# Optimization experiments

Hardware: AMD Instinct MI355X
Metric: run time of the kernel (lower is better)

Reference implementation:

```python
import jax, jax.numpy as jnp
import numpy as np

BATCH, SEQ, STATE, LATENT, ENC = 32, 2048, 64, 128, 256
INPUT_DIM = STATE + 2 * LATENT  # 320
BN_EPS = 1e-5


def setup_inputs() -> dict:
    key = jax.random.key(0)
    ks = jax.random.split(key, 16)
    def lin(k, fan_in, shape):
        b = 1.0 / np.sqrt(fan_in)
        return jax.random.uniform(k, shape, jnp.float32, -b, b)
    return {
        "padded_input": jax.random.normal(ks[0], (BATCH, SEQ, INPUT_DIM), jnp.float32),
        # encoder: state->enc, enc->enc, enc->latent (weights in (in,out) layout)
        "enc_w0": lin(ks[1], STATE, (STATE, ENC)),   "enc_b0": lin(ks[2], STATE, (ENC,)),
        "enc_w1": lin(ks[3], ENC, (ENC, ENC)),       "enc_b1": lin(ks[4], ENC, (ENC,)),
        "enc_w2": lin(ks[5], ENC, (ENC, LATENT)),    "enc_b2": lin(ks[6], ENC, (LATENT,)),
        "bn_gamma": jnp.ones((LATENT,), jnp.float32),
        "bn_beta": jnp.zeros((LATENT,), jnp.float32),
        "A_w": lin(ks[7], LATENT, (LATENT, LATENT)),  # A(x) = x @ A_w (no bias)
        "B_diag": (2.0 * jax.random.uniform(ks[8], (LATENT,), jnp.float32) - 1.0) * 0.8,
        # decoder: latent->enc, enc->enc, enc->state
        "dec_w0": lin(ks[9], LATENT, (LATENT, ENC)), "dec_b0": lin(ks[10], LATENT, (ENC,)),
        "dec_w1": lin(ks[11], ENC, (ENC, ENC)),      "dec_b1": lin(ks[12], ENC, (ENC,)),
        "dec_w2": lin(ks[13], ENC, (ENC, STATE)),    "dec_b2": lin(ks[14], ENC, (STATE,)),
        "reset_probability": 0,
        "nwarmup": 0,
    }


def reference(padded_input, enc_w0, enc_b0, enc_w1, enc_b1, enc_w2, enc_b2,
              bn_gamma, bn_beta, A_w, B_diag,
              dec_w0, dec_b0, dec_w1, dec_b1, dec_w2, dec_b2,
              reset_probability, nwarmup):
    state_dim = dec_w2.shape[1]
    latent = A_w.shape[0]
    x_t = padded_input[:, :, :state_dim]                       # [B,S,state]
    u_t1 = padded_input[:, :, state_dim + latent:]             # [B,S,latent]

    # encoder MLP (all ReLU)
    h = jax.nn.relu(x_t @ enc_w0 + enc_b0)
    h = jax.nn.relu(h @ enc_w1 + enc_b1)
    z = jax.nn.relu(h @ enc_w2 + enc_b2)                       # [B,S,latent]

    # BatchNorm1d (training mode): per-channel stats over batch and time
    mean = jnp.mean(z, axis=(0, 1))
    var = jnp.mean((z - mean) ** 2, axis=(0, 1))
    z = (z - mean) * jax.lax.rsqrt(var + BN_EPS) * bn_gamma + bn_beta

    # linear recurrence: z_0 = A z_enc[:,0] + B u_0 ; z_t = A z_{t-1} + B u_t
    d = jnp.clip(B_diag, -0.95, 0.95)
    bu = jnp.swapaxes(u_t1 * d, 0, 1)                          # [S,B,latent]

    def step(hprev, bu_t):
        hnew = hprev @ A_w + bu_t
        return hnew, hnew

    _, zs = jax.lax.scan(step, z[:, 0, :], bu)                 # [S,B,latent]
    z1 = jnp.swapaxes(zs, 0, 1)                                # [B,S,latent]

    # decoder MLP (ReLU except last)
    g = jax.nn.relu(z1 @ dec_w0 + dec_b0)
    g = jax.nn.relu(g @ dec_w1 + dec_b1)
    x_t1 = g @ dec_w2 + dec_b2                                 # [B,S,state]
    return x_t1
```

## Files before the change

### kernel.cpp

```cpp
#include <hip/hip_runtime.h>

#define DI __device__ __forceinline__

typedef __attribute__((ext_vector_type(8))) short short8;
typedef __attribute__((ext_vector_type(4))) float f32x4;
typedef unsigned short u16;
typedef unsigned int u32;

DI u16 f2bf(float f) {
  union { float f; u32 u; } v; v.f = f;
  u32 r = v.u + 0x7FFFu + ((v.u >> 16) & 1u);
  return (u16)(r >> 16);
}
DI float bf2f(u16 h) {
  union { u32 u; float f; } v; v.u = ((u32)h) << 16; return v.f;
}
DI f32x4 mfma16(short8 a, short8 b, f32x4 c) {
  return __builtin_amdgcn_mfma_f32_16x16x32_bf16(a, b, c, 0, 0, 0);
}


static const size_t OFF_HB   = 0;
static const size_t OFF_LB   = 16777216;
static const size_t OFF_WT   = 33554432;
static const size_t OFF_POWR = 34013184;
static const size_t OFF_POWT = 35127296;
static const size_t OFF_ST   = 35684352;
static const size_t OFF_ZB0  = 35685376;
static const size_t OFF_YB   = 35693568;
static const size_t OFF_INS  = 37790720;

#define OW0 0
#define OW1 16384
#define OW2 81920
#define OD0 114688
#define OD1 147456
#define OD2 212992

__global__ __launch_bounds__(256) void convw_k(const float* __restrict__ ew0, const float* __restrict__ ew1,
                                               const float* __restrict__ ew2, const float* __restrict__ dw0,
                                               const float* __restrict__ dw1, const float* __restrict__ dw2,
                                               const float* __restrict__ Aw, u16* __restrict__ wt,
                                               float* __restrict__ powR, u16* __restrict__ powT) {
  int idx = blockIdx.x * 256 + threadIdx.x;
  if (idx < 16384) { int n = idx >> 6, k = idx & 63;  wt[OW0 + idx] = f2bf(ew0[k * 256 + n]); return; }
  idx -= 16384;
  if (idx < 65536) { int n = idx >> 8, k = idx & 255; wt[OW1 + idx] = f2bf(ew1[k * 256 + n]); return; }
  idx -= 65536;
  if (idx < 32768) { int n = idx >> 8, k = idx & 255; wt[OW2 + idx] = f2bf(ew2[k * 128 + n]); return; }
  idx -= 32768;
  if (idx < 32768) { int n = idx >> 7, k = idx & 127; wt[OD0 + idx] = f2bf(dw0[k * 256 + n]); return; }
  idx -= 32768;
  if (idx < 65536) { int n = idx >> 8, k = idx & 255; wt[OD1 + idx] = f2bf(dw1[k * 256 + n]); return; }
  idx -= 65536;
  if (idx < 16384) { int n = idx >> 8, k = idx & 255; wt[OD2 + idx] = f2bf(dw2[k * 64 + n]); return; }
  idx -= 16384;
  { int k = idx >> 7, n = idx & 127;
    powR[16384 + idx] = Aw[idx];
    powT[16384 + n * 128 + k] = f2bf(Aw[idx]); }
}

template <int K, int KP, int NTW>
DI void layer(const u16* __restrict__ A, const u16* __restrict__ WT, int n0, int lm, int lq,
              f32x4 (&acc)[2][NTW]) {
  constexpr int KS = K / 32;
  constexpr int H = (KS > 4) ? 2 : 1;
  constexpr int KSH = KS / H;
#pragma unroll
  for (int h = 0; h < H; h++) {
    short8 bfr[NTW][KSH];
#pragma unroll
    for (int nt = 0; nt < NTW; nt++)
#pragma unroll
      for (int ks = 0; ks < KSH; ks++)
        bfr[nt][ks] = *(const short8*)&WT[(size_t)(n0 + nt * 16 + lm) * K + (h * KSH + ks) * 32 + lq * 8];
#pragma unroll
    for (int ks = 0; ks < KSH; ks++) {
      const int k0 = (h * KSH + ks) * 32 + lq * 8;
      short8 a0 = *(const short8*)&A[(0 * 16 + lm) * KP + k0];
      short8 a1 = *(const short8*)&A[(1 * 16 + lm) * KP + k0];
#pragma unroll
      for (int nt = 0; nt < NTW; nt++) {
        acc[0][nt] = mfma16(a0, bfr[nt][ks], acc[0][nt]);
        acc[1][nt] = mfma16(a1, bfr[nt][ks], acc[1][nt]);
      }
    }
  }
}

__global__ __launch_bounds__(256) void enc_k(const float* __restrict__ in, const u16* __restrict__ wt,
                                             const float* __restrict__ b0, const float* __restrict__ b1,
                                             const float* __restrict__ b2, float* __restrict__ st,
                                             u16* __restrict__ zb0) {
  __shared__ __align__(16) u16 bufA[32 * 264];
  __shared__ __align__(16) u16 bufB[32 * 264];
  __shared__ float sSum[128], sSq[128];
  const int tid = threadIdx.x, w = tid >> 6, l = tid & 63, lm = l & 15, lq = l >> 4;
  const int m0 = blockIdx.x * 32;
#pragma unroll
  for (int it = 0; it < 2; it++) {
    int idx = tid + it * 256;
    int row = idx >> 4, c4 = idx & 15;
    float4 f = *(const float4*)&in[(size_t)(m0 + row) * 320 + c4 * 4];
    u32 lo = (u32)f2bf(f.x) | ((u32)f2bf(f.y) << 16);
    u32 hi = (u32)f2bf(f.z) | ((u32)f2bf(f.w) << 16);
    *(uint2*)&bufA[row * 72 + c4 * 4] = make_uint2(lo, hi);
  }
  __syncthreads();
  {
    f32x4 acc[2][4];
#pragma unroll
    for (int i = 0; i < 2; i++)
#pragma unroll
      for (int j = 0; j < 4; j++) acc[i][j] = (f32x4){0.f, 0.f, 0.f, 0.f};
    layer<64, 72, 4>(bufA, wt + OW0, w * 64, lm, lq, acc);
#pragma unroll
    for (int nt = 0; nt < 4; nt++) {
      const int n = w * 64 + nt * 16 + lm;
      const float bv = b0[n];
#pragma unroll
      for (int mt = 0; mt < 2; mt++)
#pragma unroll
        for (int r = 0; r < 4; r++) {
          const int m = mt * 16 + lq * 4 + r;
          bufB[m * 264 + n] = f2bf(fmaxf(acc[mt][nt][r] + bv, 0.f));
        }
    }
  }
  __syncthreads();
  {
    f32x4 acc[2][4];
#pragma unroll
    for (int i = 0; i < 2; i++)
#pragma unroll
      for (int j = 0; j < 4; j++) acc[i][j] = (f32x4){0.f, 0.f, 0.f, 0.f};
    layer<256, 264, 4>(bufB, wt + OW1, w * 64, lm, lq, acc);
#pragma unroll
    for (int nt = 0; nt < 4; nt++) {
      const int n = w * 64 + nt * 16 + lm;
      const float bv = b1[n];
#pragma unroll
      for (int mt = 0; mt < 2; mt++)
#pragma unroll
        for (int r = 0; r < 4; r++) {
          const int m = mt * 16 + lq * 4 + r;
          bufA[m * 264 + n] = f2bf(fmaxf(acc[mt][nt][r] + bv, 0.f));
        }
    }
  }
  __syncthreads();
  {
    f32x4 acc[2][2];
#pragma unroll
    for (int i = 0; i < 2; i++)
#pragma unroll
      for (int j = 0; j < 2; j++) acc[i][j] = (f32x4){0.f, 0.f, 0.f, 0.f};
    layer<256, 264, 2>(bufA, wt + OW2, w * 32, lm, lq, acc);
    const bool t0blk = ((m0 & 2047) == 0);
#pragma unroll
    for (int nt = 0; nt < 2; nt++) {
      const int n = w * 32 + nt * 16 + lm;
      const float bv = b2[n];
      float sl = 0.f, sq = 0.f, r0v = 0.f;
#pragma unroll
      for (int mt = 0; mt < 2; mt++)
#pragma unroll
        for (int r = 0; r < 4; r++) {
          float v = fmaxf(acc[mt][nt][r] + bv, 0.f);
          sl += v; sq += v * v;
          if (mt == 0 && r == 0) r0v = v;
        }
      sl += __shfl_xor(sl, 16); sl += __shfl_xor(sl, 32);
      sq += __shfl_xor(sq, 16); sq += __shfl_xor(sq, 32);
      if (lq == 0) {
        sSum[n] = sl; sSq[n] = sq;
        if (t0blk) zb0[(m0 >> 11) * 128 + n] = f2bf(r0v);
      }
    }
  }
  __syncthreads();
  if (tid < 128) atomicAdd(&st[tid], sSum[tid]);
  else atomicAdd(&st[tid], sSq[tid - 128]);
}

__global__ __launch_bounds__(256) void dec_k(const u16* __restrict__ hb, const u16* __restrict__ wt,
                                             const float* __restrict__ b0, const float* __restrict__ b1,
                                             const float* __restrict__ b2, float* __restrict__ out) {
  __shared__ __align__(16) u16 bufA[32 * 264];
  __shared__ __align__(16) u16 bufB[32 * 264];
  const int tid = threadIdx.x, w = tid >> 6, l = tid & 63, lm = l & 15, lq = l >> 4;
  const int m0 = blockIdx.x * 32;
  for (int i = tid; i < 512; i += 256) {
    int row = i >> 4, c8 = i & 15;
    *(uint4*)&bufA[row * 136 + c8 * 8] = *(const uint4*)&hb[(size_t)(m0 + row) * 128 + c8 * 8];
  }
  __syncthreads();
  {
    f32x4 acc[2][4];
#pragma unroll
    for (int i = 0; i < 2; i++)
#pragma unroll
      for (int j = 0; j < 4; j++) acc[i][j] = (f32x4){0.f, 0.f, 0.f, 0.f};
    layer<128, 136, 4>(bufA, wt + OD0, w * 64, lm, lq, acc);
#pragma unroll
    for (int nt = 0; nt < 4; nt++) {
      const int n = w * 64 + nt * 16 + lm;
      const float bv = b0[n];
#pragma unroll
      for (int mt = 0; mt < 2; mt++)
#pragma unroll
        for (int r = 0; r < 4; r++) {
          const int m = mt * 16 + lq * 4 + r;
          bufB[m * 264 + n] = f2bf(fmaxf(acc[mt][nt][r] + bv, 0.f));
        }
    }
  }
  __syncthreads();
  {
    f32x4 acc[2][4];
#pragma unroll
    for (int i = 0; i < 2; i++)
#pragma unroll
      for (int j = 0; j < 4; j++) acc[i][j] = (f32x4){0.f, 0.f, 0.f, 0.f};
    layer<256, 264, 4>(bufB, wt + OD1, w * 64, lm, lq, acc);
#pragma unroll
    for (int nt = 0; nt < 4; nt++) {
      const int n = w * 64 + nt * 16 + lm;
      const float bv = b1[n];
#pragma unroll
      for (int mt = 0; mt < 2; mt++)
#pragma unroll
        for (int r = 0; r < 4; r++) {
          const int m = mt * 16 + lq * 4 + r;
          bufA[m * 264 + n] = f2bf(fmaxf(acc[mt][nt][r] + bv, 0.f));
        }
    }
  }
  __syncthreads();
  {
    f32x4 acc[2][1];
    acc[0][0] = (f32x4){0.f, 0.f, 0.f, 0.f};
    acc[1][0] = (f32x4){0.f, 0.f, 0.f, 0.f};
    layer<256, 264, 1>(bufA, wt + OD2, w * 16, lm, lq, acc);
    const int n = w * 16 + lm;
    const float bv = b2[n];
#pragma unroll
    for (int mt = 0; mt < 2; mt++)
#pragma unroll
      for (int r = 0; r < 4; r++) {
        const int m = mt * 16 + lq * 4 + r;
        out[(size_t)(m0 + m) * 64 + n] = acc[mt][0][r] + bv;
      }
  }
}

__global__ __launch_bounds__(128) void finalize_k(const float* __restrict__ st, const u16* __restrict__ zb0,
                                                  const float* __restrict__ gam, const float* __restrict__ bet,
                                                  u16* __restrict__ yb) {
  const int ch = threadIdx.x;
  const float mean = st[ch] * (1.f / 65536.f);
  const float var = st[128 + ch] * (1.f / 65536.f) - mean * mean;
  const float sc = rsqrtf(var + 1e-5f) * gam[ch];
  const float sh = bet[ch] - mean * sc;
  for (int b = 0; b < 32; b++) {
    float z = bf2f(zb0[b * 128 + ch]);
    yb[b * 128 + ch] = f2bf(z * sc + sh);
  }
}

__global__ __launch_bounds__(256) void pow_round_k(float* __restrict__ powR, u16* __restrict__ powT,
                                                   int p, int mi_base) {
  const int mi = mi_base + (blockIdx.x >> 2), nc = blockIdx.x & 3;
  const float* Rp = powR + (size_t)p * 16384;
  const float* Rm = powR + (size_t)(mi + 1) * 16384;
  float* Ro = powR + (size_t)(p + mi + 1) * 16384;
  u16* To = powT + (size_t)(p + mi + 1) * 16384;
  __shared__ __align__(16) float RpS[128 * 132];
  __shared__ __align__(16) float RmS[128 * 36];
  const int tid = threadIdx.x;
  for (int i = tid; i < 4096; i += 256) {
    int r = i >> 5, c4 = i & 31;
    *(float4*)&RpS[r * 132 + c4 * 4] = *(const float4*)&Rp[r * 128 + c4 * 4];
  }
  for (int i = tid; i < 1024; i += 256) {
    int r = i >> 3, c4 = i & 7;
    *(float4*)&RmS[r * 36 + c4 * 4] = *(const float4*)&Rm[r * 128 + nc * 32 + c4 * 4];
  }
  __syncthreads();
  const int tc = tid & 7, tr = tid >> 3;
  float acc[4][4];
#pragma unroll
  for (int i = 0; i < 4; i++)
#pragma unroll
    for (int j = 0; j < 4; j++) acc[i][j] = 0.f;
  for (int kk = 0; kk < 128; kk++) {
    const float4 bv = *(const float4*)&RmS[kk * 36 + tc * 4];
#pragma unroll
    for (int i = 0; i < 4; i++) {
      const float av = RpS[(tr * 4 + i) * 132 + kk];
      acc[i][0] += av * bv.x; acc[i][1] += av * bv.y;
      acc[i][2] += av * bv.z; acc[i][3] += av * bv.w;
    }
  }
#pragma unroll
  for (int i = 0; i < 4; i++)
#pragma unroll
    for (int j = 0; j < 4; j++) {
      const int row = tr * 4 + i, col = nc * 32 + tc * 4 + j;
      Ro[row * 128 + col] = acc[i][j];
      To[col * 128 + row] = f2bf(acc[i][j]);
    }
}

__global__ __launch_bounds__(256) void phase1_k(const float* __restrict__ in, const float* __restrict__ Bd,
                                                const u16* __restrict__ powT, u16* __restrict__ lb,
                                                u16* __restrict__ yb) {
  __shared__ __align__(16) u16 hS[2][32 * 136];
  __shared__ __align__(16) u16 buS[32 * 136];
  const int tid = threadIdx.x, c = blockIdx.x;
  const int w = tid >> 6, l = tid & 63, lm = l & 15, lq = l >> 4;
  const u16* T1 = powT + 16384;
  short8 bfr[2][4];
#pragma unroll
  for (int nt = 0; nt < 2; nt++)
#pragma unroll
    for (int ks = 0; ks < 4; ks++) {
      int n = (w * 2 + nt) * 16 + lm, k0 = ks * 32 + lq * 8;
      bfr[nt][ks] = *(const short8*)&T1[n * 128 + k0];
    }
  const int r0 = tid >> 4, ch = tid & 15;
  float dv[8];
#pragma unroll
  for (int j = 0; j < 8; j++) {
    float d = Bd[ch * 8 + j];
    dv[j] = fminf(0.95f, fmaxf(-0.95f, d));
  }
  const float* u0 = in + (size_t)r0 * 2048 * 320 + (size_t)(c * 8) * 320 + 192 + ch * 8;
  const float* u1 = in + (size_t)(r0 + 16) * 2048 * 320 + (size_t)(c * 8) * 320 + 192 + ch * 8;
  float4 p0 = *(const float4*)u0, p0b = *(const float4*)(u0 + 4);
  float4 p1 = *(const float4*)u1, p1b = *(const float4*)(u1 + 4);
  for (int tau = 0; tau < 8; tau++) {
    const int t = c * 8 + tau;
    short8 s0, s1;
    s0[0] = (short)f2bf(p0.x * dv[0]); s0[1] = (short)f2bf(p0.y * dv[1]);
    s0[2] = (short)f2bf(p0.z * dv[2]); s0[3] = (short)f2bf(p0.w * dv[3]);
    s0[4] = (short)f2bf(p0b.x * dv[4]); s0[5] = (short)f2bf(p0b.y * dv[5]);
    s0[6] = (short)f2bf(p0b.z * dv[6]); s0[7] = (short)f2bf(p0b.w * dv[7]);
    s1[0] = (short)f2bf(p1.x * dv[0]); s1[1] = (short)f2bf(p1.y * dv[1]);
    s1[2] = (short)f2bf(p1.z * dv[2]); s1[3] = (short)f2bf(p1.w * dv[3]);
    s1[4] = (short)f2bf(p1b.x * dv[4]); s1[5] = (short)f2bf(p1b.y * dv[5]);
    s1[6] = (short)f2bf(p1b.z * dv[6]); s1[7] = (short)f2bf(p1b.w * dv[7]);
    *(short8*)&buS[r0 * 136 + ch * 8] = s0;
    *(short8*)&buS[(r0 + 16) * 136 + ch * 8] = s1;
    __syncthreads();
    if (tau < 7) {
      const float* q0 = u0 + (tau + 1) * 320;
      const float* q1 = u1 + (tau + 1) * 320;
      p0 = *(const float4*)q0; p0b = *(const float4*)(q0 + 4);
      p1 = *(const float4*)q1; p1b = *(const float4*)(q1 + 4);
    }
    f32x4 acc[2][2];
#pragma unroll
    for (int mt = 0; mt < 2; mt++)
#pragma unroll
      for (int nt = 0; nt < 2; nt++) acc[mt][nt] = (f32x4){0.f, 0.f, 0.f, 0.f};
    if (tau > 0) {
#pragma unroll
      for (int ks = 0; ks < 4; ks++) {
        const int k0 = ks * 32 + lq * 8;
#pragma unroll
        for (int mt = 0; mt < 2; mt++) {
          short8 a = *(const short8*)&hS[tau & 1][(mt * 16 + lm) * 136 + k0];
          acc[mt][0] = mfma16(a, bfr[0][ks], acc[mt][0]);
          acc[mt][1] = mfma16(a, bfr[1][ks], acc[mt][1]);
        }
      }
    }
#pragma unroll
    for (int mt = 0; mt < 2; mt++)
#pragma unroll
      for (int nt = 0; nt < 2; nt++) {
        const int n = (w * 2 + nt) * 16 + lm;
#pragma unroll
        for (int r = 0; r < 4; r++) {
          const int m = mt * 16 + lq * 4 + r;
          float v = acc[mt][nt][r] + bf2f(buS[m * 136 + n]);
          u16 hv = f2bf(v);
          hS[(tau + 1) & 1][m * 136 + n] = hv;
          lb[((size_t)t * 32 + m) * 128 + n] = hv;
          if (tau == 7 && c < 255) yb[((size_t)(c + 1)) * 4096 + m * 128 + n] = hv;
        }
      }
    __syncthreads();
  }
}

__global__ __launch_bounds__(256) void kslf_k(const u16* __restrict__ yb, const u16* __restrict__ powT,
                                              u16* __restrict__ ins) {
  const int c = blockIdx.x, tid = threadIdx.x;
  if (c == 0) {
    for (int i = tid; i < 512; i += 256) ((uint4*)ins)[i] = ((const uint4*)yb)[i];
    return;
  }
  __shared__ __align__(16) u16 sA[32 * 136];
  __shared__ __align__(16) u16 sW[32 * 136];
  const int w = tid >> 6, l = tid & 63, lm = l & 15, lq = l >> 4;
  const u16* A8 = powT + (size_t)8 * 16384;
  short8 f8[2][4];
#pragma unroll
  for (int nt = 0; nt < 2; nt++)
#pragma unroll
    for (int ks = 0; ks < 4; ks++)
      f8[nt][ks] = *(const short8*)&A8[((w * 2 + nt) * 16 + lm) * 128 + ks * 32 + lq * 8];
  const bool havew = (c >= 2);
  if (c >= 3) {
    for (int i = tid; i < 512; i += 256) {
      int row = i >> 4, chh = i & 15;
      *(uint4*)&sA[row * 136 + chh * 8] = *(const uint4*)&yb[(size_t)(c - 3) * 4096 + row * 128 + chh * 8];
    }
    __syncthreads();
    f32x4 accw[2][2];
#pragma unroll
    for (int mt = 0; mt < 2; mt++)
#pragma unroll
      for (int nt = 0; nt < 2; nt++)
#pragma unroll
        for (int r = 0; r < 4; r++)
          accw[mt][nt][r] = bf2f(yb[(size_t)(c - 2) * 4096 + (mt * 16 + lq * 4 + r) * 128 + (w * 2 + nt) * 16 + lm]);
#pragma unroll
    for (int ks = 0; ks < 4; ks++) {
      const int k0 = ks * 32 + lq * 8;
#pragma unroll
      for (int mt = 0; mt < 2; mt++) {
        short8 a = *(const short8*)&sA[(mt * 16 + lm) * 136 + k0];
        accw[mt][0] = mfma16(a, f8[0][ks], accw[mt][0]);
        accw[mt][1] = mfma16(a, f8[1][ks], accw[mt][1]);
      }
    }
#pragma unroll
    for (int mt = 0; mt < 2; mt++)
#pragma unroll
      for (int nt = 0; nt < 2; nt++)
#pragma unroll
        for (int r = 0; r < 4; r++)
          sW[(mt * 16 + lq * 4 + r) * 136 + (w * 2 + nt) * 16 + lm] = f2bf(accw[mt][nt][r]);
  } else if (c == 2) {
    for (int i = tid; i < 512; i += 256) {
      int row = i >> 4, chh = i & 15;
      *(uint4*)&sW[row * 136 + chh * 8] = *(const uint4*)&yb[row * 128 + chh * 8];
    }
  }
  __syncthreads();
  for (int i = tid; i < 512; i += 256) {
    int row = i >> 4, chh = i & 15;
    *(uint4*)&sA[row * 136 + chh * 8] = *(const uint4*)&yb[(size_t)(c - 1) * 4096 + row * 128 + chh * 8];
  }
  __syncthreads();
  f32x4 acc[2][2];
#pragma unroll
  for (int mt = 0; mt < 2; mt++)
#pragma unroll
    for (int nt = 0; nt < 2; nt++)
#pragma unroll
      for (int r = 0; r < 4; r++)
        acc[mt][nt][r] = bf2f(yb[(size_t)c * 4096 + (mt * 16 + lq * 4 + r) * 128 + (w * 2 + nt) * 16 + lm]);
#pragma unroll
  for (int ks = 0; ks < 4; ks++) {
    const int k0 = ks * 32 + lq * 8;
#pragma unroll
    for (int mt = 0; mt < 2; mt++) {
      short8 a = *(const short8*)&sA[(mt * 16 + lm) * 136 + k0];
      acc[mt][0] = mfma16(a, f8[0][ks], acc[mt][0]);
      acc[mt][1] = mfma16(a, f8[1][ks], acc[mt][1]);
    }
  }
  if (havew) {
    const u16* A16 = powT + (size_t)16 * 16384;
    short8 f16a[2][4];
#pragma unroll
    for (int nt = 0; nt < 2; nt++)
#pragma unroll
      for (int ks = 0; ks < 4; ks++)
        f16a[nt][ks] = *(const short8*)&A16[((w * 2 + nt) * 16 + lm) * 128 + ks * 32 + lq * 8];
#pragma unroll
    for (int ks = 0; ks < 4; ks++) {
      const int k0 = ks * 32 + lq * 8;
#pragma unroll
      for (int mt = 0; mt < 2; mt++) {
        short8 a = *(const short8*)&sW[(mt * 16 + lm) * 136 + k0];
        acc[mt][0] = mfma16(a, f16a[0][ks], acc[mt][0]);
        acc[mt][1] = mfma16(a, f16a[1][ks], acc[mt][1]);
      }
    }
  }
#pragma unroll
  for (int mt = 0; mt < 2; mt++)
#pragma unroll
    for (int nt = 0; nt < 2; nt++)
#pragma unroll
      for (int r = 0; r < 4; r++)
        ins[(size_t)c * 4096 + (mt * 16 + lq * 4 + r) * 128 + (w * 2 + nt) * 16 + lm] = f2bf(acc[mt][nt][r]);
}

__global__ __launch_bounds__(256) void phase3_k(const u16* __restrict__ ins, const u16* __restrict__ powT,
                                                const u16* __restrict__ lb, u16* __restrict__ hb) {
  __shared__ __align__(16) u16 inS[32 * 136];
  const int c = blockIdx.x >> 3, tau = blockIdx.x & 7, t = c * 8 + tau;
  const int tid = threadIdx.x;
  const int w = tid >> 6, l = tid & 63, lm = l & 15, lq = l >> 4;
  const u16* Tj = powT + (size_t)(tau + 1) * 16384;
  short8 bfr[2][4];
#pragma unroll
  for (int nt = 0; nt < 2; nt++)
#pragma unroll
    for (int ks = 0; ks < 4; ks++) {
      int n = (w * 2 + nt) * 16 + lm, k0 = ks * 32 + lq * 8;
      bfr[nt][ks] = *(const short8*)&Tj[n * 128 + k0];
    }
  for (int i = tid; i < 512; i += 256) {
    int row = i >> 4, ch = i & 15;
    *(uint4*)&inS[row * 136 + ch * 8] = *(const uint4*)&ins[(size_t)c * 4096 + row * 128 + ch * 8];
  }
  __syncthreads();
  f32x4 acc[2][2];
#pragma unroll
  for (int mt = 0; mt < 2; mt++)
#pragma unroll
    for (int nt = 0; nt < 2; nt++) acc[mt][nt] = (f32x4){0.f, 0.f, 0.f, 0.f};
#pragma unroll
  for (int ks = 0; ks < 4; ks++) {
    const int k0 = ks * 32 + lq * 8;
#pragma unroll
    for (int mt = 0; mt < 2; mt++) {
      short8 a = *(const short8*)&inS[(mt * 16 + lm) * 136 + k0];
      acc[mt][0] = mfma16(a, bfr[0][ks], acc[mt][0]);
      acc[mt][1] = mfma16(a, bfr[1][ks], acc[mt][1]);
    }
  }
#pragma unroll
  for (int mt = 0; mt < 2; mt++)
#pragma unroll
    for (int nt = 0; nt < 2; nt++) {
      const int n = (w * 2 + nt) * 16 + lm;
#pragma unroll
      for (int r = 0; r < 4; r++) {
        const int m = mt * 16 + lq * 4 + r;
        float v = acc[mt][nt][r] + bf2f(lb[((size_t)t * 32 + m) * 128 + n]);
        hb[((size_t)m * 2048 + t) * 128 + n] = f2bf(v);
      }
    }
}

extern "C" void kernel_launch(void* const* d_in, const int* in_sizes, int n_in,
                              void* d_out, int out_size, void* d_ws, size_t ws_size,
                              hipStream_t stream) {
  const float* in  = (const float*)d_in[0];
  const float* ew0 = (const float*)d_in[1];  const float* eb0 = (const float*)d_in[2];
  const float* ew1 = (const float*)d_in[3];  const float* eb1 = (const float*)d_in[4];
  const float* ew2 = (const float*)d_in[5];  const float* eb2 = (const float*)d_in[6];
  const float* gam = (const float*)d_in[7];  const float* bet = (const float*)d_in[8];
  const float* Aw  = (const float*)d_in[9];  const float* Bd  = (const float*)d_in[10];
  const float* dw0 = (const float*)d_in[11]; const float* db0 = (const float*)d_in[12];
  const float* dw1 = (const float*)d_in[13]; const float* db1 = (const float*)d_in[14];
  const float* dw2 = (const float*)d_in[15]; const float* db2 = (const float*)d_in[16];

  char* ws = (char*)d_ws;
  u16*   hb   = (u16*)(ws + OFF_HB);
  u16*   lbuf = (u16*)(ws + OFF_LB);
  u16*   wt   = (u16*)(ws + OFF_WT);
  float* powR = (float*)(ws + OFF_POWR);
  u16*   powT = (u16*)(ws + OFF_POWT);
  float* st   = (float*)(ws + OFF_ST);
  u16*   zb0  = (u16*)(ws + OFF_ZB0);
  u16*   yb   = (u16*)(ws + OFF_YB);
  u16*   ins  = (u16*)(ws + OFF_INS);
  float* out  = (float*)d_out;

  hipMemsetAsync(ws + OFF_ST, 0, 1024, stream);
  convw_k<<<960, 256, 0, stream>>>(ew0, ew1, ew2, dw0, dw1, dw2, Aw, wt, powR, powT);

  pow_round_k<<<4, 256, 0, stream>>>(powR, powT, 1, 0);
  pow_round_k<<<8, 256, 0, stream>>>(powR, powT, 2, 0);
  pow_round_k<<<16, 256, 0, stream>>>(powR, powT, 4, 0);
  pow_round_k<<<4, 256, 0, stream>>>(powR, powT, 8, 7);

  phase1_k<<<256, 256, 0, stream>>>(in, Bd, powT, lbuf, yb);

  enc_k<<<2048, 256, 0, stream>>>(in, wt, eb0, eb1, eb2, st, zb0);
  finalize_k<<<1, 128, 0, stream>>>(st, zb0, gam, bet, yb);

  kslf_k<<<256, 256, 0, stream>>>(yb, powT, ins);
  phase3_k<<<2048, 256, 0, stream>>>(ins, powT, lbuf, hb);

  dec_k<<<2048, 256, 0, stream>>>(hb, wt, db0, db1, db2, out);
}
```

Baseline: 376.8 us.

## Double encoder/decoder row tile to 64 and replicate BN stat accumulators

```diff
diff --git a/kernel.cpp b/kernel.cpp
--- a/kernel.cpp
+++ b/kernel.cpp
@@ -26,9 +26,9 @@
 static const size_t OFF_POWR = 34013184;
 static const size_t OFF_POWT = 35127296;
 static const size_t OFF_ST   = 35684352;
-static const size_t OFF_ZB0  = 35685376;
-static const size_t OFF_YB   = 35693568;
-static const size_t OFF_INS  = 37790720;
+static const size_t OFF_ZB0  = 35692544;
+static const size_t OFF_YB   = 35700736;
+static const size_t OFF_INS  = 37797888;
 
 #define OW0 0
 #define OW1 16384
@@ -60,9 +60,9 @@
     powT[16384 + n * 128 + k] = f2bf(Aw[idx]); }
 }
 
-template <int K, int KP, int NTW>
+template <int K, int KP, int NTW, int MT>
 DI void layer(const u16* __restrict__ A, const u16* __restrict__ WT, int n0, int lm, int lq,
-              f32x4 (&acc)[2][NTW]) {
+              f32x4 (&acc)[MT][NTW]) {
   constexpr int KS = K / 32;
   constexpr int H = (KS > 4) ? 2 : 1;
   constexpr int KSH = KS / H;
@@ -77,30 +77,30 @@
 #pragma unroll
     for (int ks = 0; ks < KSH; ks++) {
       const int k0 = (h * KSH + ks) * 32 + lq * 8;
-      short8 a0 = *(const short8*)&A[(0 * 16 + lm) * KP + k0];
-      short8 a1 = *(const short8*)&A[(1 * 16 + lm) * KP + k0];
-#pragma unroll
-      for (int nt = 0; nt < NTW; nt++) {
-        acc[0][nt] = mfma16(a0, bfr[nt][ks], acc[0][nt]);
-        acc[1][nt] = mfma16(a1, bfr[nt][ks], acc[1][nt]);
-      }
-    }
-  }
-}
-
-__global__ __launch_bounds__(256) void enc_k(const float* __restrict__ in, const u16* __restrict__ wt,
-                                             const float* __restrict__ b0, const float* __restrict__ b1,
-                                             const float* __restrict__ b2, float* __restrict__ st,
-                                             u16* __restrict__ zb0) {
-  __shared__ __align__(16) u16 bufA[32 * 264];
-  __shared__ __align__(16) u16 bufB[32 * 264];
+      short8 a[MT];
+#pragma unroll
+      for (int mt = 0; mt < MT; mt++)
+        a[mt] = *(const short8*)&A[(mt * 16 + lm) * KP + k0];
+#pragma unroll
+      for (int nt = 0; nt < NTW; nt++)
+#pragma unroll
+        for (int mt = 0; mt < MT; mt++)
+          acc[mt][nt] = mfma16(a[mt], bfr[nt][ks], acc[mt][nt]);
+    }
+  }
+}
+
+__global__ __launch_bounds__(256, 2) void enc_k(const float* __restrict__ in, const u16* __restrict__ wt,
+                                                const float* __restrict__ b0, const float* __restrict__ b1,
+                                                const float* __restrict__ b2, float* __restrict__ st,
+                                                u16* __restrict__ zb0) {
+  __shared__ __align__(16) u16 bufA[64 * 264];
+  __shared__ __align__(16) u16 bufB[64 * 264];
   __shared__ float sSum[128], sSq[128];
   const int tid = threadIdx.x, w = tid >> 6, l = tid & 63, lm = l & 15, lq = l >> 4;
-  const int m0 = blockIdx.x * 32;
-#pragma unroll
-  for (int it = 0; it < 2; it++) {
-    int idx = tid + it * 256;
-    int row = idx >> 4, c4 = idx & 15;
+  const int m0 = blockIdx.x * 64;
+  for (int i = tid; i < 1024; i += 256) {
+    int row = i >> 4, c4 = i & 15;
     float4 f = *(const float4*)&in[(size_t)(m0 + row) * 320 + c4 * 4];
     u32 lo = (u32)f2bf(f.x) | ((u32)f2bf(f.y) << 16);
     u32 hi = (u32)f2bf(f.z) | ((u32)f2bf(f.w) << 16);
@@ -108,18 +108,19 @@
   }
   __syncthreads();
   {
-    f32x4 acc[2][4];
-#pragma unroll
-    for (int i = 0; i < 2; i++)
+    f32x4 acc[4][4];
+#pragma unroll
+    for (int i = 0; i < 4; i++)
 #pragma unroll
       for (int j = 0; j < 4; j++) acc[i][j] = (f32x4){0.f, 0.f, 0.f, 0.f};
-    layer<64, 72, 4>(bufA, wt + OW0, w * 64, lm, lq, acc);
+    layer<64, 72, 4, 4>(bufA, wt + OW0, w * 64, lm, lq, acc);
+    __syncthreads();
 #pragma unroll
     for (int nt = 0; nt < 4; nt++) {
       const int n = w * 64 + nt * 16 + lm;
       const float bv = b0[n];
 #pragma unroll
-      for (int mt = 0; mt < 2; mt++)
+      for (int mt = 0; mt < 4; mt++)
 #pragma unroll
         for (int r = 0; r < 4; r++) {
           const int m = mt * 16 + lq * 4 + r;
@@ -129,18 +130,19 @@
   }
   __syncthreads();
   {
-    f32x4 acc[2][4];
-#pragma unroll
-    for (int i = 0; i < 2; i++)
+    f32x4 acc[4][4];
+#pragma unroll
+    for (int i = 0; i < 4; i++)
 #pragma unroll
       for (int j = 0; j < 4; j++) acc[i][j] = (f32x4){0.f, 0.f, 0.f, 0.f};
-    layer<256, 264, 4>(bufB, wt + OW1, w * 64, lm, lq, acc);
+    layer<256, 264, 4, 4>(bufB, wt + OW1, w * 64, lm, lq, acc);
+    __syncthreads();
 #pragma unroll
     for (int nt = 0; nt < 4; nt++) {
       const int n = w * 64 + nt * 16 + lm;
       const float bv = b1[n];
 #pragma unroll
-      for (int mt = 0; mt < 2; mt++)
+      for (int mt = 0; mt < 4; mt++)
 #pragma unroll
         for (int r = 0; r < 4; r++) {
           const int m = mt * 16 + lq * 4 + r;
@@ -150,12 +152,12 @@
   }
   __syncthreads();
   {
-    f32x4 acc[2][2];
-#pragma unroll
-    for (int i = 0; i < 2; i++)
+    f32x4 acc[4][2];
+#pragma unroll
+    for (int i = 0; i < 4; i++)
 #pragma unroll
       for (int j = 0; j < 2; j++) acc[i][j] = (f32x4){0.f, 0.f, 0.f, 0.f};
-    layer<256, 264, 2>(bufA, wt + OW2, w * 32, lm, lq, acc);
+    layer<256, 264, 2, 4>(bufA, wt + OW2, w * 32, lm, lq, acc);
     const bool t0blk = ((m0 & 2047) == 0);
 #pragma unroll
     for (int nt = 0; nt < 2; nt++) {
@@ -163,7 +165,7 @@
       const float bv = b2[n];
       float sl = 0.f, sq = 0.f, r0v = 0.f;
 #pragma unroll
-      for (int mt = 0; mt < 2; mt++)
+      for (int mt = 0; mt < 4; mt++)
 #pragma unroll
         for (int r = 0; r < 4; r++) {
           float v = fmaxf(acc[mt][nt][r] + bv, 0.f);
@@ -179,35 +181,37 @@
     }
   }
   __syncthreads();
-  if (tid < 128) atomicAdd(&st[tid], sSum[tid]);
-  else atomicAdd(&st[tid], sSq[tid - 128]);
-}
-
-__global__ __launch_bounds__(256) void dec_k(const u16* __restrict__ hb, const u16* __restrict__ wt,
-                                             const float* __restrict__ b0, const float* __restrict__ b1,
-                                             const float* __restrict__ b2, float* __restrict__ out) {
-  __shared__ __align__(16) u16 bufA[32 * 264];
-  __shared__ __align__(16) u16 bufB[32 * 264];
+  const int rep = blockIdx.x & 7;
+  if (tid < 128) atomicAdd(&st[rep * 256 + tid], sSum[tid]);
+  else atomicAdd(&st[rep * 256 + tid], sSq[tid - 128]);
+}
+
+__global__ __launch_bounds__(256, 2) void dec_k(const u16* __restrict__ hb, const u16* __restrict__ wt,
+                                                const float* __restrict__ b0, const float* __restrict__ b1,
+                                                const float* __restrict__ b2, float* __restrict__ out) {
+  __shared__ __align__(16) u16 bufA[64 * 264];
+  __shared__ __align__(16) u16 bufB[64 * 264];
   const int tid = threadIdx.x, w = tid >> 6, l = tid & 63, lm = l & 15, lq = l >> 4;
-  const int m0 = blockIdx.x * 32;
-  for (int i = tid; i < 512; i += 256) {
+  const int m0 = blockIdx.x * 64;
+  for (int i = tid; i < 1024; i += 256) {
     int row = i >> 4, c8 = i & 15;
     *(uint4*)&bufA[row * 136 + c8 * 8] = *(const uint4*)&hb[(size_t)(m0 + row) * 128 + c8 * 8];
   }
   __syncthreads();
   {
-    f32x4 acc[2][4];
-#pragma unroll
-    for (int i = 0; i < 2; i++)
+    f32x4 acc[4][4];
+#pragma unroll
+    for (int i = 0; i < 4; i++)
 #pragma unroll
       for (int j = 0; j < 4; j++) acc[i][j] = (f32x4){0.f, 0.f, 0.f, 0.f};
-    layer<128, 136, 4>(bufA, wt + OD0, w * 64, lm, lq, acc);
+    layer<128, 136, 4, 4>(bufA, wt + OD0, w * 64, lm, lq, acc);
+    __syncthreads();
 #pragma unroll
     for (int nt = 0; nt < 4; nt++) {
       const int n = w * 64 + nt * 16 + lm;
       const float bv = b0[n];
 #pragma unroll
-      for (int mt = 0; mt < 2; mt++)
+      for (int mt = 0; mt < 4; mt++)
 #pragma unroll
         for (int r = 0; r < 4; r++) {
           const int m = mt * 16 + lq * 4 + r;
@@ -217,18 +221,19 @@
   }
   __syncthreads();
   {
-    f32x4 acc[2][4];
-#pragma unroll
-    for (int i = 0; i < 2; i++)
+    f32x4 acc[4][4];
+#pragma unroll
+    for (int i = 0; i < 4; i++)
 #pragma unroll
       for (int j = 0; j < 4; j++) acc[i][j] = (f32x4){0.f, 0.f, 0.f, 0.f};
-    layer<256, 264, 4>(bufB, wt + OD1, w * 64, lm, lq, acc);
+    layer<256, 264, 4, 4>(bufB, wt + OD1, w * 64, lm, lq, acc);
+    __syncthreads();
 #pragma unroll
     for (int nt = 0; nt < 4; nt++) {
       const int n = w * 64 + nt * 16 + lm;
       const float bv = b1[n];
 #pragma unroll
-      for (int mt = 0; mt < 2; mt++)
+      for (int mt = 0; mt < 4; mt++)
 #pragma unroll
         for (int r = 0; r < 4; r++) {
           const int m = mt * 16 + lq * 4 + r;
@@ -238,14 +243,14 @@
   }
   __syncthreads();
   {
-    f32x4 acc[2][1];
-    acc[0][0] = (f32x4){0.f, 0.f, 0.f, 0.f};
-    acc[1][0] = (f32x4){0.f, 0.f, 0.f, 0.f};
-    layer<256, 264, 1>(bufA, wt + OD2, w * 16, lm, lq, acc);
+    f32x4 acc[4][1];
+#pragma unroll
+    for (int i = 0; i < 4; i++) acc[i][0] = (f32x4){0.f, 0.f, 0.f, 0.f};
+    layer<256, 264, 1, 4>(bufA, wt + OD2, w * 16, lm, lq, acc);
     const int n = w * 16 + lm;
     const float bv = b2[n];
 #pragma unroll
-    for (int mt = 0; mt < 2; mt++)
+    for (int mt = 0; mt < 4; mt++)
 #pragma unroll
       for (int r = 0; r < 4; r++) {
         const int m = mt * 16 + lq * 4 + r;
@@ -258,8 +263,14 @@
                                                   const float* __restrict__ gam, const float* __restrict__ bet,
                                                   u16* __restrict__ yb) {
   const int ch = threadIdx.x;
-  const float mean = st[ch] * (1.f / 65536.f);
-  const float var = st[128 + ch] * (1.f / 65536.f) - mean * mean;
+  float s = 0.f, q = 0.f;
+#pragma unroll
+  for (int rep = 0; rep < 8; rep++) {
+    s += st[rep * 256 + ch];
+    q += st[rep * 256 + 128 + ch];
+  }
+  const float mean = s * (1.f / 65536.f);
+  const float var = q * (1.f / 65536.f) - mean * mean;
   const float sc = rsqrtf(var + 1e-5f) * gam[ch];
   const float sh = bet[ch] - mean * sc;
   for (int b = 0; b < 32; b++) {
@@ -576,7 +587,7 @@
   u16*   ins  = (u16*)(ws + OFF_INS);
   float* out  = (float*)d_out;
 
-  hipMemsetAsync(ws + OFF_ST, 0, 1024, stream);
+  hipMemsetAsync(ws + OFF_ST, 0, 8192, stream);
   convw_k<<<960, 256, 0, stream>>>(ew0, ew1, ew2, dw0, dw1, dw2, Aw, wt, powR, powT);
 
   pow_round_k<<<4, 256, 0, stream>>>(powR, powT, 1, 0);
@@ -586,11 +597,11 @@
 
   phase1_k<<<256, 256, 0, stream>>>(in, Bd, powT, lbuf, yb);
 
-  enc_k<<<2048, 256, 0, stream>>>(in, wt, eb0, eb1, eb2, st, zb0);
+  enc_k<<<1024, 256, 0, stream>>>(in, wt, eb0, eb1, eb2, st, zb0);
   finalize_k<<<1, 128, 0, stream>>>(st, zb0, gam, bet, yb);
 
   kslf_k<<<256, 256, 0, stream>>>(yb, powT, ins);
   phase3_k<<<2048, 256, 0, stream>>>(ins, powT, lbuf, hb);
 
-  dec_k<<<2048, 256, 0, stream>>>(hb, wt, db0, db1, db2, out);
-}
+  dec_k<<<1024, 256, 0, stream>>>(hb, wt, db0, db1, db2, out);
+}
```

Measured after the change: 308.0 us. 18.3% less time.
